# Optimization experiments

Hardware: AMD Instinct MI355X
Metric: run time of the kernel (lower is better)

## Reference

```python
import jax, jax.numpy as jnp
import numpy as np

NUM_CAMERAS = 16
IN_SIZE = 256
OUT_SIZE = 128
BATCH = 8192


def setup_inputs() -> dict:
    key = jax.random.key(0)
    k1, k2, k3, k4 = jax.random.split(key, 4)
    x = jax.random.normal(k1, (BATCH, IN_SIZE), dtype=jnp.float32)
    cam = jax.random.randint(k2, (BATCH,), 0, NUM_CAMERAS, dtype=jnp.int64)
    # Per-camera Linear params, torch-style init U(-1/sqrt(in), 1/sqrt(in))
    bound = 1.0 / np.sqrt(IN_SIZE)
    W = jax.random.uniform(k3, (NUM_CAMERAS, OUT_SIZE, IN_SIZE), dtype=jnp.float32, minval=-bound, maxval=bound)
    b = jax.random.uniform(k4, (NUM_CAMERAS, OUT_SIZE), dtype=jnp.float32, minval=-bound, maxval=bound)
    return {"x": x, "cam": cam, "W": W, "b": b}


def reference(x, cam, W, b):
    # Per-sample expert linear: y_b = W[cam_b] @ x_b + b[cam_b], then sigmoid.
    Wg = W[cam]            # [B, out, in] gathered per-sample weights
    bg = b[cam]            # [B, out]
    y = jnp.einsum('bi,boi->bo', x, Wg) + bg
    return jax.nn.sigmoid(y)
```

## Files before the change

kernel.cpp:

```cpp
#include <hip/hip_runtime.h>
#include <hip/hip_bf16.h>

#define NCAM   16
#define IN     256
#define OUT    128
#define BATCH  8192
#define NSLICE 32
#define SLICE  (BATCH / NSLICE)
#define OHALF  64
#define XROW   (IN + 8)

typedef short bfx8 __attribute__((ext_vector_type(8)));
typedef short bfx4 __attribute__((ext_vector_type(4)));
typedef float fx4  __attribute__((ext_vector_type(4)));

__device__ inline short f2bf(float f) {
    __hip_bfloat16 h = __float2bfloat16(f);
    return *reinterpret_cast<short*>(&h);
}

__device__ inline float sigmoidf(float v) {
    return 1.0f / (1.0f + __expf(-v));
}

__global__ __launch_bounds__(256, 3) void fc_expert_kernel(
    const float* __restrict__ x,
    const int*   __restrict__ cam,
    const float* __restrict__ W,
    const float* __restrict__ bias,
    float*       __restrict__ out)
{
    __shared__ int   s_list[SLICE];
    __shared__ int   s_cnt[4];
    __shared__ short __align__(16) s_w[OHALF * XROW];
    __shared__ short __align__(16) s_x[16 * XROW];

    const int slice = blockIdx.x;
    const int c     = blockIdx.y;
    const int obase = blockIdx.z * OHALF;
    const int tid   = threadIdx.x;
    const int lane  = tid & 63;
    const int w     = tid >> 6;
    const int base  = slice * SLICE;

    const int oq   = lane & 15;
    const int quad = lane >> 4;

    const int g0  = base + w * 64 + lane;
    const int myc = cam[g0];

    const float* wp = W + (size_t)(c * OUT + obase + w * 16) * IN;
    fx4 wv[16];
    #pragma unroll
    for (int i = 0; i < 16; ++i)
        wv[i] = *(const fx4*)(wp + (size_t)i * IN + lane * 4);

    const float bo = bias[c * OUT + obase + w * 16 + oq];

    const bool f = (myc == c);
    const unsigned long long mask = __ballot(f);
    if (lane == 0) s_cnt[w] = __popcll(mask);
    __syncthreads();
    int off = 0;
    #pragma unroll
    for (int ww = 0; ww < 4; ++ww) off += (ww < w) ? s_cnt[ww] : 0;
    const int m = s_cnt[0] + s_cnt[1] + s_cnt[2] + s_cnt[3];
    const int pre = __popcll(mask & ((1ull << lane) - 1ull));
    if (f) s_list[off + pre] = g0;

    #pragma unroll
    for (int i = 0; i < 16; ++i) {
        fx4 v = wv[i];
        bfx4 sv;
        sv[0] = f2bf(v[0]); sv[1] = f2bf(v[1]); sv[2] = f2bf(v[2]); sv[3] = f2bf(v[3]);
        *(bfx4*)(s_w + (w * 16 + i) * XROW + lane * 4) = sv;
    }
    __syncthreads();

    for (int cb = 0; cb < m; cb += 16) {
        #pragma unroll
        for (int rr = 0; rr < 4; ++rr) {
            int row = rr * 4 + w;
            int li  = cb + row;
            bfx4 sv;
            if (li < m) {
                int g = s_list[li];
                fx4 v = *(const fx4*)(x + (size_t)g * IN + lane * 4);
                sv[0] = f2bf(v[0]); sv[1] = f2bf(v[1]); sv[2] = f2bf(v[2]); sv[3] = f2bf(v[3]);
            } else {
                sv[0] = 0; sv[1] = 0; sv[2] = 0; sv[3] = 0;
            }
            *(bfx4*)(s_x + row * XROW + lane * 4) = sv;
        }
        __syncthreads();

        fx4 acc = {0.f, 0.f, 0.f, 0.f};
        #pragma unroll
        for (int kk = 0; kk < 8; ++kk) {
            bfx8 a = *(const bfx8*)(s_x + oq * XROW + kk * 32 + quad * 8);
            bfx8 b = *(const bfx8*)(s_w + (w * 16 + oq) * XROW + kk * 32 + quad * 8);
            acc = __builtin_amdgcn_mfma_f32_16x16x32_bf16(a, b, acc, 0, 0, 0);
        }

        #pragma unroll
        for (int r = 0; r < 4; ++r) {
            int srow = quad * 4 + r;
            if (cb + srow < m) {
                int g = s_list[cb + srow];
                out[(size_t)g * OUT + obase + w * 16 + oq] = sigmoidf(acc[r] + bo);
            }
        }
        __syncthreads();
    }
}

extern "C" void kernel_launch(void* const* d_in, const int* in_sizes, int n_in,
                              void* d_out, int out_size, void* d_ws, size_t ws_size,
                              hipStream_t stream) {
    const float* x    = (const float*)d_in[0];
    const int*   cam  = (const int*)d_in[1];
    const float* W    = (const float*)d_in[2];
    const float* bias = (const float*)d_in[3];
    float* out = (float*)d_out;

    dim3 grid(NSLICE, NCAM, 2);
    fc_expert_kernel<<<grid, 256, 0, stream>>>(x, cam, W, bias, out);
}
```

Measured before the change: 74.30 us.

## Split into bf16 prep kernel and chunked per-camera GEMM with direct-to-LDS loads

Adds a prep kernel that converts x and W to bf16 once and builds a compact per-camera sample list with a prefix scan. The GEMM kernel then processes 64-sample chunks per camera, loading swizzled bf16 tiles straight into LDS with global_load_lds. Each wave keeps its W fragment in registers across four MFMA subtiles. This removes the repeated fp32 W reloads, the per-block cam scans and conversions, and the 16-row inner loop. In exchange it adds a second launch, an extra pass over x through the workspace, and a fixed list cap of 1024 samples per camera.

After: 81.73 us. 10.0% more time.

```diff
diff --git a/kernel.cpp b/kernel.cpp
--- a/kernel.cpp
+++ b/kernel.cpp
@@ -1,17 +1,19 @@
 #include <hip/hip_runtime.h>
 #include <hip/hip_bf16.h>
 
-#define NCAM   16
-#define IN     256
-#define OUT    128
-#define BATCH  8192
-#define NSLICE 32
-#define SLICE  (BATCH / NSLICE)
-#define OHALF  64
-#define XROW   (IN + 8)
+#define NCAM    16
+#define IN      256
+#define OUT     128
+#define BATCH   8192
+#define LISTCAP 1024
+#define CHUNK   64
+#define NCHUNK  (LISTCAP / CHUNK)
+
+#define CONV_W_ITEMS (NCAM * OUT * IN / 8)
+#define CONV_X_ITEMS (BATCH * IN / 8)
+#define NBLKA (NCAM + (CONV_W_ITEMS + CONV_X_ITEMS) / 256)
 
 typedef short bfx8 __attribute__((ext_vector_type(8)));
-typedef short bfx4 __attribute__((ext_vector_type(4)));
 typedef float fx4  __attribute__((ext_vector_type(4)));
 
 __device__ inline short f2bf(float f) {
@@ -23,94 +25,146 @@
     return 1.0f / (1.0f + __expf(-v));
 }
 
-__global__ __launch_bounds__(256, 3) void fc_expert_kernel(
+typedef const __attribute__((address_space(1))) unsigned int* gptr_t;
+typedef __attribute__((address_space(3))) unsigned int* lptr_t;
+
+__device__ inline void glds16(const void* g, void* l) {
+    __builtin_amdgcn_global_load_lds((gptr_t)g, (lptr_t)l, 16, 0, 0);
+}
+
+__global__ __launch_bounds__(256) void prep_kernel(
     const float* __restrict__ x,
     const int*   __restrict__ cam,
     const float* __restrict__ W,
+    short*       __restrict__ xb,
+    short*       __restrict__ wb,
+    int*         __restrict__ cnt,
+    int*         __restrict__ lists)
+{
+    const int tid = threadIdx.x;
+    const int b   = blockIdx.x;
+
+    if (b < NCAM) {
+        __shared__ int pc[256];
+        const int c = b;
+        int cl = 0;
+        for (int j = tid; j < BATCH; j += 256) cl += (cam[j] == c);
+        pc[tid] = cl;
+        __syncthreads();
+        for (int s = 1; s < 256; s <<= 1) {
+            int v = (tid >= s) ? pc[tid - s] : 0;
+            __syncthreads();
+            pc[tid] += v;
+            __syncthreads();
+        }
+        if (tid == 255) cnt[c] = pc[255];
+        int pos = pc[tid] - cl;
+        for (int j = tid; j < BATCH; j += 256) {
+            if (cam[j] == c) {
+                if (pos < LISTCAP) lists[c * LISTCAP + pos] = j;
+                ++pos;
+            }
+        }
+    } else {
+        int idx = (b - NCAM) * 256 + tid;
+        const float* src;
+        short* dst;
+        if (idx < CONV_W_ITEMS) {
+            src = W  + (size_t)idx * 8;
+            dst = wb + (size_t)idx * 8;
+        } else {
+            idx -= CONV_W_ITEMS;
+            src = x  + (size_t)idx * 8;
+            dst = xb + (size_t)idx * 8;
+        }
+        fx4 v0 = *(const fx4*)(src);
+        fx4 v1 = *(const fx4*)(src + 4);
+        bfx8 o;
+        o[0] = f2bf(v0[0]); o[1] = f2bf(v0[1]); o[2] = f2bf(v0[2]); o[3] = f2bf(v0[3]);
+        o[4] = f2bf(v1[0]); o[5] = f2bf(v1[1]); o[6] = f2bf(v1[2]); o[7] = f2bf(v1[3]);
+        *(bfx8*)dst = o;
+    }
+}
+
+__global__ __launch_bounds__(256, 2) void gemm_kernel(
+    const short* __restrict__ xb,
+    const short* __restrict__ wb,
     const float* __restrict__ bias,
+    const int*   __restrict__ cnt,
+    const int*   __restrict__ lists,
     float*       __restrict__ out)
 {
-    __shared__ int   s_list[SLICE];
-    __shared__ int   s_cnt[4];
-    __shared__ short __align__(16) s_w[OHALF * XROW];
-    __shared__ short __align__(16) s_x[16 * XROW];
+    __shared__ short __align__(16) s_x[CHUNK * IN];
+    __shared__ short __align__(16) s_w[CHUNK * IN];
+    __shared__ int s_list[CHUNK];
 
-    const int slice = blockIdx.x;
+    const int chunk = blockIdx.x;
     const int c     = blockIdx.y;
-    const int obase = blockIdx.z * OHALF;
+    const int obase = blockIdx.z * 64;
     const int tid   = threadIdx.x;
     const int lane  = tid & 63;
     const int w     = tid >> 6;
-    const int base  = slice * SLICE;
+    const int oq    = lane & 15;
+    const int quad  = lane >> 4;
 
-    const int oq   = lane & 15;
-    const int quad = lane >> 4;
+    const int nc   = cnt[c];
+    const int base = chunk * CHUNK;
+    if (base >= nc) return;
+    const int m = min(CHUNK, nc - base);
 
-    const int g0  = base + w * 64 + lane;
-    const int myc = cam[g0];
+    const int half = lane >> 5;
+    const int cidx = lane & 31;
 
-    const float* wp = W + (size_t)(c * OUT + obase + w * 16) * IN;
-    fx4 wv[16];
+    const short* wsrc = wb + (size_t)(c * OUT + obase) * IN;
     #pragma unroll
-    for (int i = 0; i < 16; ++i)
-        wv[i] = *(const fx4*)(wp + (size_t)i * IN + lane * 4);
+    for (int i = 0; i < 8; ++i) {
+        int r  = w * 16 + i * 2 + half;
+        int cs = cidx ^ (r & 7);
+        glds16(wsrc + (size_t)r * IN + cs * 8, s_w + (w * 16 + i * 2) * IN);
+    }
+
+    const int* lst = lists + c * LISTCAP + base;
+    if (tid < CHUNK) s_list[tid] = lst[min(tid, m - 1)];
+
+    #pragma unroll
+    for (int i = 0; i < 8; ++i) {
+        int r  = w * 16 + i * 2 + half;
+        int g  = lst[min(r, m - 1)];
+        int cs = cidx ^ (r & 7);
+        glds16(xb + (size_t)g * IN + cs * 8, s_x + (w * 16 + i * 2) * IN);
+    }
 
     const float bo = bias[c * OUT + obase + w * 16 + oq];
+    __syncthreads();
 
-    const bool f = (myc == c);
-    const unsigned long long mask = __ballot(f);
-    if (lane == 0) s_cnt[w] = __popcll(mask);
-    __syncthreads();
-    int off = 0;
+    bfx8 bf[8];
     #pragma unroll
-    for (int ww = 0; ww < 4; ++ww) off += (ww < w) ? s_cnt[ww] : 0;
-    const int m = s_cnt[0] + s_cnt[1] + s_cnt[2] + s_cnt[3];
-    const int pre = __popcll(mask & ((1ull << lane) - 1ull));
-    if (f) s_list[off + pre] = g0;
+    for (int kk = 0; kk < 8; ++kk) {
+        int cs = (kk * 4 + quad) ^ (oq & 7);
+        bf[kk] = *(const bfx8*)(s_w + (w * 16 + oq) * IN + cs * 8);
+    }
+    fx4 zero = {0.f, 0.f, 0.f, 0.f};
+    fx4 acc[4] = {zero, zero, zero, zero};
+    #pragma unroll
+    for (int st = 0; st < 4; ++st) {
+        #pragma unroll
+        for (int kk = 0; kk < 8; ++kk) {
+            int cs = (kk * 4 + quad) ^ (oq & 7);
+            bfx8 a = *(const bfx8*)(s_x + (st * 16 + oq) * IN + cs * 8);
+            acc[st] = __builtin_amdgcn_mfma_f32_16x16x32_bf16(a, bf[kk], acc[st], 0, 0, 0);
+        }
+    }
 
     #pragma unroll
-    for (int i = 0; i < 16; ++i) {
-        fx4 v = wv[i];
-        bfx4 sv;
-        sv[0] = f2bf(v[0]); sv[1] = f2bf(v[1]); sv[2] = f2bf(v[2]); sv[3] = f2bf(v[3]);
-        *(bfx4*)(s_w + (w * 16 + i) * XROW + lane * 4) = sv;
-    }
-    __syncthreads();
-
-    for (int cb = 0; cb < m; cb += 16) {
-        #pragma unroll
-        for (int rr = 0; rr < 4; ++rr) {
-            int row = rr * 4 + w;
-            int li  = cb + row;
-            bfx4 sv;
-            if (li < m) {
-                int g = s_list[li];
-                fx4 v = *(const fx4*)(x + (size_t)g * IN + lane * 4);
-                sv[0] = f2bf(v[0]); sv[1] = f2bf(v[1]); sv[2] = f2bf(v[2]); sv[3] = f2bf(v[3]);
-            } else {
-                sv[0] = 0; sv[1] = 0; sv[2] = 0; sv[3] = 0;
-            }
-            *(bfx4*)(s_x + row * XROW + lane * 4) = sv;
-        }
-        __syncthreads();
-
-        fx4 acc = {0.f, 0.f, 0.f, 0.f};
-        #pragma unroll
-        for (int kk = 0; kk < 8; ++kk) {
-            bfx8 a = *(const bfx8*)(s_x + oq * XROW + kk * 32 + quad * 8);
-            bfx8 b = *(const bfx8*)(s_w + (w * 16 + oq) * XROW + kk * 32 + quad * 8);
-            acc = __builtin_amdgcn_mfma_f32_16x16x32_bf16(a, b, acc, 0, 0, 0);
-        }
-
+    for (int st = 0; st < 4; ++st) {
         #pragma unroll
         for (int r = 0; r < 4; ++r) {
-            int srow = quad * 4 + r;
-            if (cb + srow < m) {
-                int g = s_list[cb + srow];
-                out[(size_t)g * OUT + obase + w * 16 + oq] = sigmoidf(acc[r] + bo);
+            int s = st * 16 + quad * 4 + r;
+            if (s < m) {
+                int g = s_list[s];
+                out[(size_t)g * OUT + obase + w * 16 + oq] = sigmoidf(acc[st][r] + bo);
             }
         }
-        __syncthreads();
     }
 }
 
@@ -123,6 +177,12 @@
     const float* bias = (const float*)d_in[3];
     float* out = (float*)d_out;
 
-    dim3 grid(NSLICE, NCAM, 2);
-    fc_expert_kernel<<<grid, 256, 0, stream>>>(x, cam, W, bias, out);
+    char* ws = (char*)d_ws;
+    short* xb  = (short*)ws;
+    short* wb  = (short*)(ws + (size_t)BATCH * IN * 2);
+    int*   cnt = (int*)(ws + (size_t)BATCH * IN * 2 + (size_t)NCAM * OUT * IN * 2);
+    int*   lists = cnt + 64;
+
+    prep_kernel<<<dim3(NBLKA), 256, 0, stream>>>(x, cam, W, xb, wb, cnt, lists);
+    gemm_kernel<<<dim3(NCHUNK, NCAM, 2), 256, 0, stream>>>(xb, wb, bias, cnt, lists, out);
 }
```

## Enlarge batch slices and tiles to reuse per-camera weights across more samples

Applied to the files above, without the earlier changes.

Cuts the number of batch slices and doubles the block to 512 threads. Each block now gathers about four times as many matching samples and processes them in 64-row chunks, with the weight MFMA fragments kept in registers. This reduces redundant loading and bf16 conversion of the per-camera weight tiles, which dominated memory traffic. The cost is fewer blocks (roughly one per CU), so there is less parallelism and latency hiding.

Measured after the change: 74.75 us. No clear change (+0.6%).

```diff
diff --git a/kernel.cpp b/kernel.cpp
--- a/kernel.cpp
+++ b/kernel.cpp
@@ -5,10 +5,11 @@
 #define IN     256
 #define OUT    128
 #define BATCH  8192
-#define NSLICE 32
+#define NSLICE 8
 #define SLICE  (BATCH / NSLICE)
 #define OHALF  64
 #define XROW   (IN + 8)
+#define CHUNK  64
 
 typedef short bfx8 __attribute__((ext_vector_type(8)));
 typedef short bfx4 __attribute__((ext_vector_type(4)));
@@ -23,7 +24,7 @@
     return 1.0f / (1.0f + __expf(-v));
 }
 
-__global__ __launch_bounds__(256, 3) void fc_expert_kernel(
+__global__ __launch_bounds__(512, 2) void fc_expert_kernel(
     const float* __restrict__ x,
     const int*   __restrict__ cam,
     const float* __restrict__ W,
@@ -31,9 +32,9 @@
     float*       __restrict__ out)
 {
     __shared__ int   s_list[SLICE];
-    __shared__ int   s_cnt[4];
+    __shared__ int   s_cnt[16];
     __shared__ short __align__(16) s_w[OHALF * XROW];
-    __shared__ short __align__(16) s_x[16 * XROW];
+    __shared__ short __align__(16) s_x[CHUNK * XROW];
 
     const int slice = blockIdx.x;
     const int c     = blockIdx.y;
@@ -41,73 +42,88 @@
     const int tid   = threadIdx.x;
     const int lane  = tid & 63;
     const int w     = tid >> 6;
+    const int w4    = w & 3;
     const int base  = slice * SLICE;
+    const int oq    = lane & 15;
+    const int quad  = lane >> 4;
 
-    const int oq   = lane & 15;
-    const int quad = lane >> 4;
+    const int g0 = base + w * 128 + lane;
+    const int g1 = g0 + 64;
+    const int c0 = cam[g0];
+    const int c1 = cam[g1];
 
-    const int g0  = base + w * 64 + lane;
-    const int myc = cam[g0];
+    const float* wp = W + (size_t)(c * OUT + obase) * IN;
+    fx4 wv[8];
+    #pragma unroll
+    for (int i = 0; i < 8; ++i)
+        wv[i] = *(const fx4*)(wp + (size_t)(w + 8 * i) * IN + lane * 4);
 
-    const float* wp = W + (size_t)(c * OUT + obase + w * 16) * IN;
-    fx4 wv[16];
-    #pragma unroll
-    for (int i = 0; i < 16; ++i)
-        wv[i] = *(const fx4*)(wp + (size_t)i * IN + lane * 4);
+    const float bo = bias[c * OUT + obase + w4 * 16 + oq];
 
-    const float bo = bias[c * OUT + obase + w * 16 + oq];
-
-    const bool f = (myc == c);
-    const unsigned long long mask = __ballot(f);
-    if (lane == 0) s_cnt[w] = __popcll(mask);
-    __syncthreads();
-    int off = 0;
-    #pragma unroll
-    for (int ww = 0; ww < 4; ++ww) off += (ww < w) ? s_cnt[ww] : 0;
-    const int m = s_cnt[0] + s_cnt[1] + s_cnt[2] + s_cnt[3];
-    const int pre = __popcll(mask & ((1ull << lane) - 1ull));
-    if (f) s_list[off + pre] = g0;
+    const bool f0 = (c0 == c), f1 = (c1 == c);
+    const unsigned long long b0 = __ballot(f0);
+    const unsigned long long b1 = __ballot(f1);
+    if (lane == 0) { s_cnt[w * 2] = __popcll(b0); s_cnt[w * 2 + 1] = __popcll(b1); }
 
     #pragma unroll
-    for (int i = 0; i < 16; ++i) {
+    for (int i = 0; i < 8; ++i) {
         fx4 v = wv[i];
         bfx4 sv;
         sv[0] = f2bf(v[0]); sv[1] = f2bf(v[1]); sv[2] = f2bf(v[2]); sv[3] = f2bf(v[3]);
-        *(bfx4*)(s_w + (w * 16 + i) * XROW + lane * 4) = sv;
+        *(bfx4*)(s_w + (w + 8 * i) * XROW + lane * 4) = sv;
     }
     __syncthreads();
 
-    for (int cb = 0; cb < m; cb += 16) {
+    int off0 = 0, mtot = 0;
+    #pragma unroll
+    for (int k = 0; k < 16; ++k) {
+        int v = s_cnt[k];
+        off0 += (k < w * 2) ? v : 0;
+        mtot += v;
+    }
+    const int m = mtot;
+    const unsigned long long pm = (1ull << lane) - 1ull;
+    if (f0) s_list[off0 + __popcll(b0 & pm)] = g0;
+    if (f1) s_list[off0 + __popcll(b0) + __popcll(b1 & pm)] = g1;
+
+    bfx8 bfrag[8];
+    #pragma unroll
+    for (int kk = 0; kk < 8; ++kk)
+        bfrag[kk] = *(const bfx8*)(s_w + (w4 * 16 + oq) * XROW + kk * 32 + quad * 8);
+
+    __syncthreads();
+
+    for (int cb = 0; cb < m; cb += CHUNK) {
         #pragma unroll
-        for (int rr = 0; rr < 4; ++rr) {
-            int row = rr * 4 + w;
+        for (int j = 0; j < 8; ++j) {
+            int row = w + 8 * j;
             int li  = cb + row;
-            bfx4 sv;
+            bfx4 sv = {0, 0, 0, 0};
             if (li < m) {
                 int g = s_list[li];
                 fx4 v = *(const fx4*)(x + (size_t)g * IN + lane * 4);
                 sv[0] = f2bf(v[0]); sv[1] = f2bf(v[1]); sv[2] = f2bf(v[2]); sv[3] = f2bf(v[3]);
-            } else {
-                sv[0] = 0; sv[1] = 0; sv[2] = 0; sv[3] = 0;
             }
             *(bfx4*)(s_x + row * XROW + lane * 4) = sv;
         }
         __syncthreads();
 
-        fx4 acc = {0.f, 0.f, 0.f, 0.f};
         #pragma unroll
-        for (int kk = 0; kk < 8; ++kk) {
-            bfx8 a = *(const bfx8*)(s_x + oq * XROW + kk * 32 + quad * 8);
-            bfx8 b = *(const bfx8*)(s_w + (w * 16 + oq) * XROW + kk * 32 + quad * 8);
-            acc = __builtin_amdgcn_mfma_f32_16x16x32_bf16(a, b, acc, 0, 0, 0);
-        }
-
-        #pragma unroll
-        for (int r = 0; r < 4; ++r) {
-            int srow = quad * 4 + r;
-            if (cb + srow < m) {
-                int g = s_list[cb + srow];
-                out[(size_t)g * OUT + obase + w * 16 + oq] = sigmoidf(acc[r] + bo);
+        for (int u = 0; u < 2; ++u) {
+            int t = (w >> 2) * 2 + u;
+            fx4 acc = {0.f, 0.f, 0.f, 0.f};
+            #pragma unroll
+            for (int kk = 0; kk < 8; ++kk) {
+                bfx8 a = *(const bfx8*)(s_x + (t * 16 + oq) * XROW + kk * 32 + quad * 8);
+                acc = __builtin_amdgcn_mfma_f32_16x16x32_bf16(a, bfrag[kk], acc, 0, 0, 0);
+            }
+            #pragma unroll
+            for (int r = 0; r < 4; ++r) {
+                int s = cb + t * 16 + quad * 4 + r;
+                if (s < m) {
+                    int g = s_list[s];
+                    out[(size_t)g * OUT + obase + w4 * 16 + oq] = sigmoidf(acc[r] + bo);
+                }
             }
         }
         __syncthreads();
@@ -124,5 +140,5 @@
     float* out = (float*)d_out;
 
     dim3 grid(NSLICE, NCAM, 2);
-    fc_expert_kernel<<<grid, 256, 0, stream>>>(x, cam, W, bias, out);
+    fc_expert_kernel<<<grid, 512, 0, stream>>>(x, cam, W, bias, out);
 }
```
